# Kernel optimization log

Measured on AMD Instinct MI355X. Metric: run time of the kernel, lower is better.

## Reference

```python
import jax, jax.numpy as jnp
import numpy as np

N_HEADS = 4
N_HIDDEN = 256  # out_features with concat=False
SLOPE = 0.1
NEG_INF = -9e15


def setup_inputs() -> dict:
    key = jax.random.key(0)
    k1, k2, k3, k4 = jax.random.split(key, 4)
    N, F_IN = 4096, 512
    h = jax.random.normal(k1, (N, F_IN), dtype=jnp.float32)
    adj_mat = jax.random.randint(k2, (N, N), 0, 2, dtype=jnp.int32)
    # xavier_normal gain=1.414
    W = jax.random.normal(k3, (F_IN, N_HIDDEN * N_HEADS), dtype=jnp.float32) * (
        1.414 * np.sqrt(2.0 / (F_IN + N_HIDDEN * N_HEADS)))
    a = jax.random.normal(k4, (N_HEADS, 2 * N_HIDDEN, 1), dtype=jnp.float32) * (
        1.414 * np.sqrt(2.0 / (2 * N_HIDDEN + 1)))
    return {"h": h, "adj_mat": adj_mat, "W": W, "a": a}


def reference(h, adj_mat, W, a):
    N = h.shape[0]
    # [N, H*D] -> [H, N, D]
    ht = (h @ W).reshape(N, N_HEADS, N_HIDDEN).transpose(1, 0, 2)
    lr = jax.nn.leaky_relu(ht, SLOPE)
    # additive attention: a split into source/target halves
    src = jnp.einsum('hnd,hd->hn', lr, a[:, :N_HIDDEN, 0])   # [H, N]
    tgt = jnp.einsum('hnd,hd->hn', lr, a[:, N_HIDDEN:, 0])   # [H, N]
    e = src[:, :, None] + tgt[:, None, :]                    # [H, N, N]
    e = jnp.where(adj_mat > 0, e, NEG_INF)
    attn = jax.nn.softmax(e, axis=-1)
    out = jnp.einsum('hnm,hmd->hnd', attn, ht)               # [H, N, D]
    return out.mean(axis=0)                                  # concat=False -> mean over heads
```

## Files before the change

kernel.cpp:

```cpp
#include <hip/hip_runtime.h>

#define N_NODES 4096
#define F_IN 512
#define NHID 256
#define HD 1024
#define NPAD 1152

typedef _Float16 half8 __attribute__((ext_vector_type(8)));
typedef _Float16 half4 __attribute__((ext_vector_type(4)));
typedef float floatx4 __attribute__((ext_vector_type(4)));
typedef float float4v __attribute__((ext_vector_type(4)));
typedef int int4v __attribute__((ext_vector_type(4)));
typedef unsigned int uint4v __attribute__((ext_vector_type(4)));

__device__ __forceinline__ float bf2f(unsigned short u) {
  union { unsigned int i; float f; } x; x.i = ((unsigned int)u) << 16; return x.f;
}

__device__ __forceinline__ void async_copy16(const void* g, void* l) {
  __builtin_amdgcn_global_load_lds((const __attribute__((address_space(1))) void*)g,
                                   (__attribute__((address_space(3))) void*)l, 16, 0, 0);
}

__global__ void detect_kernel(const unsigned short* __restrict__ hbits, int* __restrict__ flag) {
  const int t = threadIdx.x;
  int cnt = 0;
  for (int i = t; i < 1024; i += 256) {
    int e = (hbits[i] >> 7) & 0xFF;
    cnt += (e >= 115 && e <= 135) ? 1 : 0;
  }
  __shared__ int red[256];
  red[t] = cnt; __syncthreads();
  for (int s = 128; s > 0; s >>= 1) { if (t < s) red[t] += red[t + s]; __syncthreads(); }
  if (t == 0) flag[0] = (red[0] >= 900) ? 1 : 0;
}

template <typename OutT>
__global__ __launch_bounds__(256) void gemm_bt(
    const _Float16* __restrict__ A, const _Float16* __restrict__ BT,
    OutT* __restrict__ C, int K, int ldc, int klen, long csz)
{
  __shared__ _Float16 sA[2][128 * 32];
  __shared__ _Float16 sB[2][128 * 32];

  const int nbx = gridDim.x, nby = gridDim.y;
  const int total = nbx * nby * gridDim.z;
  int lin = blockIdx.x + nbx * (blockIdx.y + nby * blockIdx.z);
  int tile;
  if ((total & 7) == 0) {
    tile = (lin & 7) * (total >> 3) + (lin >> 3);
  } else {
    tile = lin;
  }
  const int n_idx = tile % nbx;
  const int rem   = tile / nbx;
  const int m_idx = rem % nby;
  const int kz    = rem / nby;

  const int n0 = n_idx * 128;
  const int m0 = m_idx * 128;
  const int kbeg = kz * klen;
  const int kend = kbeg + klen;
  OutT* Cz = C + (long)kz * csz;

  const int t = threadIdx.x;
  const int w = t >> 6;
  const int lane = t & 63;
  const int wm = (w >> 1) << 6;
  const int wn = (w & 1) << 6;

  floatx4 acc[4][4] = {};

  const int l4 = lane >> 2;
  const int kk = (lane & 3) << 3;
  const int c0 = w << 1;

  const _Float16* gA = A + (long)m0 * K;
  const _Float16* gBT = BT + (long)n0 * K;

  const int koff = (lane >> 4) << 3;
  const int rA = wm + (lane & 15);
  const int rB = wn + (lane & 15);

  auto STAGE = [&](int buf, int k0) {
#pragma unroll
    for (int p = 0; p < 2; ++p) {
      const int c = c0 + p;
      const int row = c * 16 + l4;
      async_copy16(gA + (long)row * K + k0 + kk, &sA[buf][c * 512 + lane * 8]);
      async_copy16(gBT + (long)row * K + k0 + kk, &sB[buf][c * 512 + lane * 8]);
    }
  };

  STAGE(0, kbeg);
  __syncthreads();

  int cur = 0;
  for (int k0 = kbeg; k0 < kend; k0 += 32) {
    if (k0 + 32 < kend) STAGE(cur ^ 1, k0 + 32);

    half8 af[4], bf[4];
#pragma unroll
    for (int i = 0; i < 4; ++i)
      af[i] = *(const half8*)&sA[cur][(rA + i * 16) * 32 + koff];
#pragma unroll
    for (int i = 0; i < 4; ++i)
      bf[i] = *(const half8*)&sB[cur][(rB + i * 16) * 32 + koff];
#pragma unroll
    for (int i = 0; i < 4; ++i)
#pragma unroll
      for (int j = 0; j < 4; ++j)
        acc[i][j] = __builtin_amdgcn_mfma_f32_16x16x32_f16(af[i], bf[j], acc[i][j], 0, 0, 0);

    __syncthreads();
    cur ^= 1;
  }

  const int q4 = (lane >> 4) << 2;
#pragma unroll
  for (int i = 0; i < 4; ++i) {
#pragma unroll
    for (int j = 0; j < 4; ++j) {
      const int gr = m0 + wm + i * 16 + q4;
      const int gc = n0 + wn + j * 16 + (lane & 15);
#pragma unroll
      for (int r = 0; r < 4; ++r)
        Cz[(long)(gr + r) * ldc + gc] = (OutT)acc[i][j][r];
    }
  }
}

__global__ void cvt_h_kernel(const void* __restrict__ in, _Float16* __restrict__ out,
                             const int* __restrict__ flag, int n8) {
  int i = blockIdx.x * 256 + threadIdx.x;
  if (i >= n8) return;
  half8 o;
  if (*flag) {
    union { uint4v v; unsigned short s[8]; } u;
    u.v = ((const uint4v*)in)[i];
#pragma unroll
    for (int e = 0; e < 8; ++e) o[e] = (_Float16)bf2f(u.s[e]);
  } else {
    const float4v* f = (const float4v*)in + 2 * i;
    float4v x0 = f[0], x1 = f[1];
#pragma unroll
    for (int e = 0; e < 4; ++e) { o[e] = (_Float16)x0[e]; o[4 + e] = (_Float16)x1[e]; }
  }
  ((half8*)out)[i] = o;
}

__global__ void cvt_adj_kernel(const int* __restrict__ adj, _Float16* __restrict__ out, int n8) {
  int i = blockIdx.x * 256 + threadIdx.x;
  if (i >= n8) return;
  int4v A = ((const int4v*)adj)[2 * i];
  int4v B = ((const int4v*)adj)[2 * i + 1];
  half8 o;
#pragma unroll
  for (int e = 0; e < 4; ++e) {
    o[e]     = (_Float16)(A[e] > 0 ? 1.0f : 0.0f);
    o[4 + e] = (_Float16)(B[e] > 0 ? 1.0f : 0.0f);
  }
  ((half8*)out)[i] = o;
}

__global__ void cvt_a_kernel(const void* __restrict__ a, float* __restrict__ aF,
                             const int* __restrict__ flag) {
  const int t = threadIdx.x;
  const int bf = *flag;
#pragma unroll
  for (int e = 0; e < 8; ++e) {
    int idx = t * 8 + e;
    aF[idx] = bf ? bf2f(((const unsigned short*)a)[idx]) : ((const float*)a)[idx];
  }
}

__global__ void transpose_w_kernel(const void* __restrict__ W, _Float16* __restrict__ WT,
                                   const int* __restrict__ flag) {
  __shared__ _Float16 tile[64][72];
  const int k0 = blockIdx.x * 64, n0 = blockIdx.y * 64;
  const int t = threadIdx.x, r = t >> 3, c = t & 7;
  const int bf = *flag;
#pragma unroll
  for (int q = 0; q < 2; ++q) {
    int k = r + q * 32;
    half8 v;
    if (bf) {
      union { uint4v vv; unsigned short s[8]; } u;
      u.vv = *(const uint4v*)&((const unsigned short*)W)[(long)(k0 + k) * HD + n0 + c * 8];
#pragma unroll
      for (int e = 0; e < 8; ++e) v[e] = (_Float16)bf2f(u.s[e]);
    } else {
      const float4v* f = (const float4v*)&((const float*)W)[(long)(k0 + k) * HD + n0 + c * 8];
      float4v x0 = f[0], x1 = f[1];
#pragma unroll
      for (int e = 0; e < 4; ++e) { v[e] = (_Float16)x0[e]; v[4 + e] = (_Float16)x1[e]; }
    }
    *(half8*)&tile[k][c * 8] = v;
  }
  __syncthreads();
#pragma unroll
  for (int q = 0; q < 2; ++q) {
    int n = r + q * 32;
    half8 o;
#pragma unroll
    for (int e = 0; e < 8; ++e) o[e] = tile[c * 8 + e][n];
    *(half8*)&WT[(long)(n0 + n) * F_IN + k0 + c * 8] = o;
  }
}

__global__ void tgt_kernel(const _Float16* __restrict__ ht, const float* __restrict__ aF,
                           float* __restrict__ tgt) {
  const int i = blockIdx.x;
  const int t = threadIdx.x, h = t >> 6, lane = t & 63;
  half4 v = *(const half4*)&ht[(long)i * HD + h * NHID + lane * 4];
  float4v av = *(const float4v*)&aF[h * 512 + NHID + lane * 4];
  float s = 0.f;
#pragma unroll
  for (int e = 0; e < 4; ++e) {
    float x = (float)v[e];
    x = x > 0.f ? x : 0.1f * x;
    s += x * av[e];
  }
#pragma unroll
  for (int o = 32; o > 0; o >>= 1) s += __shfl_down(s, o);
  if (lane == 0) tgt[h * N_NODES + i] = s;
}

__global__ void maxexp_kernel(const float* __restrict__ tgt, float* __restrict__ wbuf,
                              _Float16* __restrict__ VT) {
  const int h = blockIdx.x, t = threadIdx.x;
  const float* row = tgt + h * N_NODES;
  float4v v[4];
  float m = -3.0e38f;
#pragma unroll
  for (int q = 0; q < 4; ++q) {
    v[q] = *(const float4v*)&row[(t + q * 256) * 4];
#pragma unroll
    for (int e = 0; e < 4; ++e) m = fmaxf(m, v[q][e]);
  }
#pragma unroll
  for (int o = 32; o > 0; o >>= 1) m = fmaxf(m, __shfl_down(m, o));
  __shared__ float red[4];
  if ((t & 63) == 0) red[t >> 6] = m;
  __syncthreads();
  m = fmaxf(fmaxf(red[0], red[1]), fmaxf(red[2], red[3]));
#pragma unroll
  for (int q = 0; q < 4; ++q) {
    const int j0 = (t + q * 256) * 4;
    float4v wv;
#pragma unroll
    for (int e = 0; e < 4; ++e) wv[e] = __expf(v[q][e] - m);
    *(float4v*)&wbuf[h * N_NODES + j0] = wv;
    half4 hv;
#pragma unroll
    for (int e = 0; e < 4; ++e) hv[e] = (_Float16)wv[e];
    *(half4*)&VT[(long)(HD + h) * N_NODES + j0] = hv;
  }
}

__global__ void scaled_transpose_kernel(const _Float16* __restrict__ ht, const float* __restrict__ wbuf,
                                        _Float16* __restrict__ VT) {
  __shared__ _Float16 tile[64][72];
  const int j0 = blockIdx.x * 64, n0 = blockIdx.y * 64;
  const int t = threadIdx.x, r = t >> 3, c = t & 7;
#pragma unroll
  for (int q = 0; q < 2; ++q) {
    int j = r + q * 32;
    *(half8*)&tile[j][c * 8] = *(const half8*)&ht[(long)(j0 + j) * HD + n0 + c * 8];
  }
  __syncthreads();
  const int h = n0 >> 8;
  const float* wrow = wbuf + h * N_NODES + j0;
#pragma unroll
  for (int q = 0; q < 2; ++q) {
    int n = r + q * 32;
    half8 o;
#pragma unroll
    for (int e = 0; e < 8; ++e) {
      int j = c * 8 + e;
      o[e] = (_Float16)(wrow[j] * (float)tile[j][n]);
    }
    *(half8*)&VT[(long)(n0 + n) * N_NODES + j0 + c * 8] = o;
  }
}

__global__ void epilogue_kernel(const float* __restrict__ S, float* __restrict__ out, int ns) {
  const int i = blockIdx.x, d = threadIdx.x;
  const long SZ = (long)N_NODES * NPAD;
  float num[4] = {0.f, 0.f, 0.f, 0.f};
  float den[4] = {0.f, 0.f, 0.f, 0.f};
  for (int z = 0; z < ns; ++z) {
    const float* row = S + z * SZ + (long)i * NPAD;
#pragma unroll
    for (int h = 0; h < 4; ++h) {
      num[h] += row[h * NHID + d];
      den[h] += row[HD + h];
    }
  }
  float r = 0.f;
#pragma unroll
  for (int h = 0; h < 4; ++h) r += num[h] / den[h];
  out[(long)i * NHID + d] = 0.25f * r;
}

extern "C" void kernel_launch(void* const* d_in, const int* in_sizes, int n_in,
                              void* d_out, int out_size, void* d_ws, size_t ws_size,
                              hipStream_t stream) {
  const void* h = nullptr; const int* adj = nullptr; const void* W = nullptr; const void* a = nullptr;
  for (int i = 0; i < n_in; ++i) {
    switch (in_sizes[i]) {
      case 2097152:  h   = d_in[i]; break;
      case 16777216: adj = (const int*)d_in[i]; break;
      case 524288:   W   = d_in[i]; break;
      case 2048:     a   = d_in[i]; break;
      default: break;
    }
  }
  float* out = (float*)d_out;

  char* ws = (char*)d_ws;
  const size_t OFF_ADJF = 0;
  const size_t OFF_VT   = 33554432;
  const size_t OFF_TGT  = OFF_VT + 9437184;
  const size_t OFF_WBUF = OFF_TGT + 65536;
  const size_t OFF_M    = OFF_WBUF + 65536;
  const size_t OFF_AF   = OFF_M + 256;
  const size_t OFF_X    = OFF_AF + 8192;
  const size_t SPART    = 18874368;

  int ns = 1;
  if      (ws_size >= OFF_X + 4 * SPART) ns = 4;
  else if (ws_size >= OFF_X + 2 * SPART) ns = 2;
  if (ws_size < OFF_X + SPART || !h || !adj || !W || !a) return;

  _Float16* adjF = (_Float16*)(ws + OFF_ADJF);
  _Float16* VT   = (_Float16*)(ws + OFF_VT);
  float*    tgt  = (float*)(ws + OFF_TGT);
  float*    wbuf = (float*)(ws + OFF_WBUF);
  int*      flag = (int*)(ws + OFF_M + 32);
  float*    aF   = (float*)(ws + OFF_AF);
  _Float16* hF = (_Float16*)(ws + OFF_X);
  _Float16* WT = (_Float16*)(ws + OFF_X + 4194304);
  _Float16* ht = (_Float16*)(ws + OFF_X + 5242880);
  float*    S  = (float*)(ws + OFF_X);

  detect_kernel<<<1, 256, 0, stream>>>((const unsigned short*)h, flag);
  cvt_h_kernel<<<1024, 256, 0, stream>>>(h, hF, flag, 262144);
  cvt_adj_kernel<<<8192, 256, 0, stream>>>(adj, adjF, 2097152);
  cvt_a_kernel<<<1, 256, 0, stream>>>(a, aF, flag);
  transpose_w_kernel<<<dim3(8, 16), 256, 0, stream>>>(W, WT, flag);
  gemm_bt<_Float16><<<dim3(8, 32, 1), 256, 0, stream>>>(hF, WT, ht, F_IN, HD, F_IN, 0);
  tgt_kernel<<<4096, 256, 0, stream>>>(ht, aF, tgt);
  maxexp_kernel<<<4, 256, 0, stream>>>(tgt, wbuf, VT);
  scaled_transpose_kernel<<<dim3(64, 16), 256, 0, stream>>>(ht, wbuf, VT);
  gemm_bt<float><<<dim3(9, 32, ns), 256, 0, stream>>>(adjF, VT, S, N_NODES, NPAD,
                                                      N_NODES / ns, (long)N_NODES * NPAD);
  epilogue_kernel<<<4096, 256, 0, stream>>>(S, out, ns);
}
```

Before: 217.7 us.

## Fuse adjacency conversion into projection GEMM launch and swizzle GEMM LDS layout

Merges the adjacency int-to-half conversion into the same launch as the h@W projection GEMM. The first 256 blocks run the GEMM and the remaining blocks convert adjacency, so the small GEMM grid overlaps with the memory-bound conversion and one launch is removed. It also XOR-swizzles the K offsets in both the global-to-LDS copies and the LDS fragment reads to reduce shared-memory bank conflicts in both GEMMs. The fused kernel allocates LDS for every block, including the conversion blocks, which may limit occupancy for the conversion part.

```diff
diff --git a/kernel.cpp b/kernel.cpp
--- a/kernel.cpp
+++ b/kernel.cpp
@@ -36,22 +36,13 @@
 }
 
 template <typename OutT>
-__global__ __launch_bounds__(256) void gemm_bt(
+__device__ __forceinline__ void gemm_core(
     const _Float16* __restrict__ A, const _Float16* __restrict__ BT,
-    OutT* __restrict__ C, int K, int ldc, int klen, long csz)
+    OutT* __restrict__ C, int K, int ldc, int klen, long csz,
+    int lin, int nbx, int nby, int total,
+    _Float16* __restrict__ sA, _Float16* __restrict__ sB)
 {
-  __shared__ _Float16 sA[2][128 * 32];
-  __shared__ _Float16 sB[2][128 * 32];
-
-  const int nbx = gridDim.x, nby = gridDim.y;
-  const int total = nbx * nby * gridDim.z;
-  int lin = blockIdx.x + nbx * (blockIdx.y + nby * blockIdx.z);
-  int tile;
-  if ((total & 7) == 0) {
-    tile = (lin & 7) * (total >> 3) + (lin >> 3);
-  } else {
-    tile = lin;
-  }
+  int tile = ((total & 7) == 0) ? ((lin & 7) * (total >> 3) + (lin >> 3)) : lin;
   const int n_idx = tile % nbx;
   const int rem   = tile / nbx;
   const int m_idx = rem % nby;
@@ -72,13 +63,13 @@
   floatx4 acc[4][4] = {};
 
   const int l4 = lane >> 2;
-  const int kk = (lane & 3) << 3;
+  const int kksw = (((lane & 3) ^ ((lane >> 2) & 3)) << 3);
   const int c0 = w << 1;
 
   const _Float16* gA = A + (long)m0 * K;
   const _Float16* gBT = BT + (long)n0 * K;
 
-  const int koff = (lane >> 4) << 3;
+  const int rsw = (((lane >> 4) ^ (lane & 3)) << 3);
   const int rA = wm + (lane & 15);
   const int rB = wn + (lane & 15);
 
@@ -87,8 +78,8 @@
     for (int p = 0; p < 2; ++p) {
       const int c = c0 + p;
       const int row = c * 16 + l4;
-      async_copy16(gA + (long)row * K + k0 + kk, &sA[buf][c * 512 + lane * 8]);
-      async_copy16(gBT + (long)row * K + k0 + kk, &sB[buf][c * 512 + lane * 8]);
+      async_copy16(gA + (long)row * K + k0 + kksw, &sA[buf * 4096 + c * 512 + lane * 8]);
+      async_copy16(gBT + (long)row * K + k0 + kksw, &sB[buf * 4096 + c * 512 + lane * 8]);
     }
   };
 
@@ -102,10 +93,10 @@
     half8 af[4], bf[4];
 #pragma unroll
     for (int i = 0; i < 4; ++i)
-      af[i] = *(const half8*)&sA[cur][(rA + i * 16) * 32 + koff];
+      af[i] = *(const half8*)&sA[cur * 4096 + (rA + i * 16) * 32 + rsw];
 #pragma unroll
     for (int i = 0; i < 4; ++i)
-      bf[i] = *(const half8*)&sB[cur][(rB + i * 16) * 32 + koff];
+      bf[i] = *(const half8*)&sB[cur * 4096 + (rB + i * 16) * 32 + rsw];
 #pragma unroll
     for (int i = 0; i < 4; ++i)
 #pragma unroll
@@ -127,6 +118,43 @@
       for (int r = 0; r < 4; ++r)
         Cz[(long)(gr + r) * ldc + gc] = (OutT)acc[i][j][r];
     }
+  }
+}
+
+template <typename OutT>
+__global__ __launch_bounds__(256) void gemm_bt(
+    const _Float16* __restrict__ A, const _Float16* __restrict__ BT,
+    OutT* __restrict__ C, int K, int ldc, int klen, long csz)
+{
+  __shared__ _Float16 sA[2 * 128 * 32];
+  __shared__ _Float16 sB[2 * 128 * 32];
+  const int nbx = gridDim.x, nby = gridDim.y;
+  const int total = nbx * nby * gridDim.z;
+  const int lin = blockIdx.x + nbx * (blockIdx.y + nby * blockIdx.z);
+  gemm_core<OutT>(A, BT, C, K, ldc, klen, csz, lin, nbx, nby, total, sA, sB);
+}
+
+__global__ __launch_bounds__(256) void fused_ht_cvt_kernel(
+    const _Float16* __restrict__ hF, const _Float16* __restrict__ WT,
+    _Float16* __restrict__ ht, const int* __restrict__ adj,
+    _Float16* __restrict__ adjF)
+{
+  __shared__ _Float16 sA[2 * 128 * 32];
+  __shared__ _Float16 sB[2 * 128 * 32];
+  const int b = blockIdx.x;
+  if (b < 256) {
+    gemm_core<_Float16>(hF, WT, ht, F_IN, HD, F_IN, 0, b, 8, 32, 256, sA, sB);
+  } else {
+    const int i = (b - 256) * 256 + threadIdx.x;
+    int4v A = ((const int4v*)adj)[2 * i];
+    int4v B = ((const int4v*)adj)[2 * i + 1];
+    half8 o;
+#pragma unroll
+    for (int e = 0; e < 4; ++e) {
+      o[e]     = (_Float16)(A[e] > 0 ? 1.0f : 0.0f);
+      o[4 + e] = (_Float16)(B[e] > 0 ? 1.0f : 0.0f);
+    }
+    ((half8*)adjF)[i] = o;
   }
 }
 
@@ -145,20 +173,6 @@
     float4v x0 = f[0], x1 = f[1];
 #pragma unroll
     for (int e = 0; e < 4; ++e) { o[e] = (_Float16)x0[e]; o[4 + e] = (_Float16)x1[e]; }
-  }
-  ((half8*)out)[i] = o;
-}
-
-__global__ void cvt_adj_kernel(const int* __restrict__ adj, _Float16* __restrict__ out, int n8) {
-  int i = blockIdx.x * 256 + threadIdx.x;
-  if (i >= n8) return;
-  int4v A = ((const int4v*)adj)[2 * i];
-  int4v B = ((const int4v*)adj)[2 * i + 1];
-  half8 o;
-#pragma unroll
-  for (int e = 0; e < 4; ++e) {
-    o[e]     = (_Float16)(A[e] > 0 ? 1.0f : 0.0f);
-    o[4 + e] = (_Float16)(B[e] > 0 ? 1.0f : 0.0f);
   }
   ((half8*)out)[i] = o;
 }
@@ -346,10 +360,9 @@
 
   detect_kernel<<<1, 256, 0, stream>>>((const unsigned short*)h, flag);
   cvt_h_kernel<<<1024, 256, 0, stream>>>(h, hF, flag, 262144);
-  cvt_adj_kernel<<<8192, 256, 0, stream>>>(adj, adjF, 2097152);
   cvt_a_kernel<<<1, 256, 0, stream>>>(a, aF, flag);
   transpose_w_kernel<<<dim3(8, 16), 256, 0, stream>>>(W, WT, flag);
-  gemm_bt<_Float16><<<dim3(8, 32, 1), 256, 0, stream>>>(hF, WT, ht, F_IN, HD, F_IN, 0);
+  fused_ht_cvt_kernel<<<8448, 256, 0, stream>>>(hF, WT, ht, adj, adjF);
   tgt_kernel<<<4096, 256, 0, stream>>>(ht, aF, tgt);
   maxexp_kernel<<<4, 256, 0, stream>>>(tgt, wbuf, VT);
   scaled_transpose_kernel<<<dim3(64, 16), 256, 0, stream>>>(ht, wbuf, VT);
```

After: 212.1 us. 2.6% less time.
